# Optimization experiments

Hardware: AMD Instinct MI355X
Metric: run time of the kernel (lower is better)

## Reference

```python
import jax, jax.numpy as jnp
import numpy as np

N_NODES = 50000
N_EDGES = 800000
IN_C = 128
HID = 128
OUT_C = 64
N_GRAPHS = 256


def setup_inputs() -> dict:
    key = jax.random.key(0)
    ks = jax.random.split(key, 12)
    x = jax.random.normal(ks[0], (N_NODES, IN_C), dtype=jnp.float32)
    edge_index = jax.random.randint(ks[1], (2, N_EDGES), 0, N_NODES, dtype=jnp.int32)
    batch = jnp.sort(jax.random.randint(ks[2], (N_NODES,), 0, N_GRAPHS, dtype=jnp.int32))
    def lin(k, fan_in, fan_out):
        bound = 1.0 / np.sqrt(fan_in)
        kw, kb = jax.random.split(k)
        W = jax.random.uniform(kw, (fan_in, fan_out), minval=-bound, maxval=bound, dtype=jnp.float32)
        b = jax.random.uniform(kb, (fan_out,), minval=-bound, maxval=bound, dtype=jnp.float32)
        return W, b
    W1a, b1a = lin(ks[3], IN_C, HID)
    W1b, b1b = lin(ks[4], HID, HID)
    W2a, b2a = lin(ks[5], HID, HID)
    W2b, b2b = lin(ks[6], HID, HID)
    Wl, bl = lin(ks[7], HID, OUT_C)
    return {"x": x, "edge_index": edge_index, "batch": batch,
            "W1a": W1a, "b1a": b1a, "W1b": W1b, "b1b": b1b,
            "W2a": W2a, "b2a": b2a, "W2b": W2b, "b2b": b2b,
            "Wl": Wl, "bl": bl}


def gin_conv(x, edge_index, Wa, ba, Wb, bb):
    # GINConv with eps=0: h_i = MLP(x_i + sum_{j->i} x_j)
    src, dst = edge_index[0], edge_index[1]
    agg = jax.ops.segment_sum(x[src], dst, num_segments=x.shape[0])  # [N, d]
    h = x + agg
    h = jax.nn.relu(h @ Wa + ba) @ Wb + bb
    return h


def reference(x, edge_index, batch, W1a, b1a, W1b, b1b, W2a, b2a, W2b, b2b, Wl, bl):
    h = gin_conv(x, edge_index, W1a, b1a, W1b, b1b)
    h = gin_conv(h, edge_index, W2a, b2a, W2b, b2b)
    # global mean pool over graphs in the batch
    sums = jax.ops.segment_sum(h, batch, num_segments=N_GRAPHS)          # [G, HID]
    cnts = jax.ops.segment_sum(jnp.ones((h.shape[0],), h.dtype), batch, num_segments=N_GRAPHS)
    pooled = sums / jnp.maximum(cnts, 1.0)[:, None]
    return pooled @ Wl + bl  # [G, OUT_C]
```

## Files before the change

### kernel.cpp

```cpp
#include <hip/hip_runtime.h>

constexpr int N  = 50000;
constexpr int E  = 800000;
constexpr int C  = 128;
constexpr int G  = 256;
constexpr int OC = 64;
constexpr int D  = 64;

constexpr int NBUCK = 196;
constexpr int BCAP  = 5120;
constexpr int EPB = 2048;
constexpr int EB  = (E + EPB - 1) / EPB;
constexpr int WB1 = 64;
constexpr int WXB = 64;
constexpr int WHB = 32;
constexpr int GB  = (N + 255) / 256;
constexpr int FB  = NBUCK;
constexpr int MB  = (N + 63) / 64;

typedef __attribute__((ext_vector_type(8))) short short8;
typedef __attribute__((ext_vector_type(4))) float f32x4;
typedef __attribute__((ext_vector_type(2))) float f32x2;

__device__ __forceinline__ unsigned int au(float f) { return __float_as_uint(f); }

__device__ __forceinline__ unsigned short f2bf(float f) {
    unsigned int u = au(f);
    u += 0x7fffu + ((u >> 16) & 1u);
    return (unsigned short)(u >> 16);
}
__device__ __forceinline__ unsigned int pack_bf16(float lo, float hi) {
    return ((au(hi) + 0x8000u) & 0xFFFF0000u) | ((au(lo) + 0x8000u) >> 16);
}

__device__ __forceinline__ void acc16(f32x2* a, uint4 v) {
    a[0] += __builtin_amdgcn_cvt_pk_f32_fp8((int)v.x, false);
    a[1] += __builtin_amdgcn_cvt_pk_f32_fp8((int)v.x, true);
    a[2] += __builtin_amdgcn_cvt_pk_f32_fp8((int)v.y, false);
    a[3] += __builtin_amdgcn_cvt_pk_f32_fp8((int)v.y, true);
    a[4] += __builtin_amdgcn_cvt_pk_f32_fp8((int)v.z, false);
    a[5] += __builtin_amdgcn_cvt_pk_f32_fp8((int)v.z, true);
    a[6] += __builtin_amdgcn_cvt_pk_f32_fp8((int)v.w, false);
    a[7] += __builtin_amdgcn_cvt_pk_f32_fp8((int)v.w, true);
}
__device__ __forceinline__ void set16(f32x2* a, uint4 v) {
    a[0] = __builtin_amdgcn_cvt_pk_f32_fp8((int)v.x, false);
    a[1] = __builtin_amdgcn_cvt_pk_f32_fp8((int)v.x, true);
    a[2] = __builtin_amdgcn_cvt_pk_f32_fp8((int)v.y, false);
    a[3] = __builtin_amdgcn_cvt_pk_f32_fp8((int)v.y, true);
    a[4] = __builtin_amdgcn_cvt_pk_f32_fp8((int)v.z, false);
    a[5] = __builtin_amdgcn_cvt_pk_f32_fp8((int)v.z, true);
    a[6] = __builtin_amdgcn_cvt_pk_f32_fp8((int)v.w, false);
    a[7] = __builtin_amdgcn_cvt_pk_f32_fp8((int)v.w, true);
}

__device__ __forceinline__ void gather_rows(f32x2* a, const uint4* F16,
                                            const unsigned short* irow, int dg, int l) {
    const uint2* i2 = (const uint2*)irow;
    int nb  = dg >> 2;
    int rem = dg & 3;
    if (nb > 0) {
        uint2 iu = i2[0];
        int t0 = (int)(iu.x & 0xffffu), t1 = (int)(iu.x >> 16);
        int t2 = (int)(iu.y & 0xffffu), t3 = (int)(iu.y >> 16);
        uint4 v0 = F16[(size_t)t0 * 8 + l];
        uint4 v1 = F16[(size_t)t1 * 8 + l];
        uint4 v2 = F16[(size_t)t2 * 8 + l];
        uint4 v3 = F16[(size_t)t3 * 8 + l];
        for (int b = 1; b < nb; ++b) {
            uint2 ju = i2[b];
            int u0 = (int)(ju.x & 0xffffu), u1 = (int)(ju.x >> 16);
            int u2 = (int)(ju.y & 0xffffu), u3 = (int)(ju.y >> 16);
            uint4 w0 = F16[(size_t)u0 * 8 + l];
            uint4 w1 = F16[(size_t)u1 * 8 + l];
            uint4 w2 = F16[(size_t)u2 * 8 + l];
            uint4 w3 = F16[(size_t)u3 * 8 + l];
            acc16(a, v0); acc16(a, v1); acc16(a, v2); acc16(a, v3);
            v0 = w0; v1 = w1; v2 = w2; v3 = w3;
        }
        acc16(a, v0); acc16(a, v1); acc16(a, v2); acc16(a, v3);
    }
    if (rem) {
        const unsigned short* ir = irow + nb * 4;
#pragma unroll
        for (int m = 0; m < 3; ++m) {
            if (m < rem) {
                uint4 v = F16[(size_t)ir[m] * 8 + l];
                acc16(a, v);
            }
        }
    }
}

__device__ __forceinline__ void tile_sort(short* sorted, const int* deg, int row0,
                                          int lane, int wave) {
    if (wave == 0) {
        int n0 = row0 + lane;
        int key = (n0 < N) ? min(deg[n0], D) : -1;
        int rank = 0;
        for (int j = 0; j < 64; ++j) {
            int kj = __shfl(key, j);
            rank += (kj < key) || (kj == key && j < lane);
        }
        sorted[rank] = (short)lane;
    }
}


__global__ __launch_bounds__(256) void build_prep_kernel(const int* __restrict__ src,
                                                         const int* __restrict__ dst,
                                                         int* __restrict__ bcount,
                                                         unsigned int* __restrict__ bucketbuf,
                                                         const float* __restrict__ W1a,
                                                         const float* __restrict__ W1b,
                                                         const float* __restrict__ W2a,
                                                         const float* __restrict__ W2b,
                                                         const float* __restrict__ Wl,
                                                         const float* __restrict__ bl,
                                                         const float* __restrict__ b1b,
                                                         const float* __restrict__ b2b,
                                                         unsigned short* __restrict__ wt1a,
                                                         unsigned short* __restrict__ wtx,
                                                         float* __restrict__ Whead,
                                                         float* __restrict__ c1,
                                                         float* __restrict__ bhead,
                                                         const int* __restrict__ batch,
                                                         int* __restrict__ gcnt) {
    int b = blockIdx.x;
    int tid = threadIdx.x;
    if (b < EB) {
        __shared__ int lcount[NBUCK];
        __shared__ int lbase[NBUCK];
        __shared__ int lcur[NBUCK];
        for (int i = tid; i < NBUCK; i += 256) { lcount[i] = 0; lcur[i] = 0; }
        __syncthreads();
        int e0 = b * EPB;
        int sv[8], dv[8];
#pragma unroll
        for (int i = 0; i < 8; ++i) {
            int e = e0 + i * 256 + tid;
            if (e < E) {
                sv[i] = src[e];
                dv[i] = dst[e];
                atomicAdd(&lcount[dv[i] >> 8], 1);
            } else {
                dv[i] = -1;
            }
        }
        __syncthreads();
        if (tid < NBUCK) {
            int c = lcount[tid];
            lbase[tid] = (c > 0) ? atomicAdd(&bcount[tid], c) : 0;
        }
        __syncthreads();
#pragma unroll
        for (int i = 0; i < 8; ++i) {
            if (dv[i] >= 0) {
                int bk = dv[i] >> 8;
                int pos = lbase[bk] + atomicAdd(&lcur[bk], 1);
                if (pos < BCAP)
                    bucketbuf[(size_t)bk * BCAP + pos] =
                        ((unsigned int)sv[i] << 16) | (unsigned int)(dv[i] & 255);
            }
        }
    } else if (b < EB + WB1) {
        int idx = (b - EB) * 256 + tid;
        int n = idx >> 7, k = idx & 127;
        wt1a[idx] = f2bf(W1a[k * 128 + n]);
    } else if (b < EB + WB1 + WXB) {
        int idx = (b - EB - WB1) * 256 + tid;
        int i = idx >> 7, j = idx & 127;
        float acc = 0.f;
        for (int k = 0; k < 128; ++k) acc += W1b[i * 128 + k] * W2a[k * 128 + j];
        wtx[j * 128 + i] = f2bf(acc);
    } else if (b < EB + WB1 + WXB + WHB) {
        int idx = (b - EB - WB1 - WXB) * 256 + tid;
        int i = idx >> 6, j = idx & 63;
        float acc = 0.f;
        for (int k = 0; k < 128; ++k) acc += W2b[i * 128 + k] * Wl[k * OC + j];
        Whead[i * OC + j] = acc;
    } else if (b == EB + WB1 + WXB + WHB) {
        if (tid < 128) {
            float acc = 0.f;
            for (int k = 0; k < 128; ++k) acc += b1b[k] * W2a[k * 128 + tid];
            c1[tid] = acc;
        } else if (tid < 192) {
            int j = tid - 128;
            float acc = bl[j];
            for (int k = 0; k < 128; ++k) acc += b2b[k] * Wl[k * OC + j];
            bhead[j] = acc;
        }
    } else {
        __shared__ int h[G];
        h[tid] = 0;
        __syncthreads();
        int i = (b - (EB + WB1 + WXB + WHB + 1)) * 256 + tid;
        if (i < N) atomicAdd(&h[batch[i]], 1);
        __syncthreads();
        int c = h[tid];
        if (c > 0) atomicAdd(&gcnt[tid], c);
    }
}


__global__ __launch_bounds__(512, 6) void mid_kernel(const int* __restrict__ bcount,
                                                     const unsigned int* __restrict__ bucketbuf,
                                                     unsigned short* __restrict__ ell,
                                                     int* __restrict__ deg,
                                                     const float* __restrict__ x,
                                                     const unsigned short* __restrict__ wt1a,
                                                     unsigned char* __restrict__ z1) {
    int tid = threadIdx.x;
    if (blockIdx.x < FB) {
        __shared__ int lcur[256];
        int b = blockIdx.x;
        if (tid < 256) lcur[tid] = 0;
        __syncthreads();
        int cnt = min(bcount[b], BCAP);
        const unsigned int* buf = bucketbuf + (size_t)b * BCAP;
        int nbase = b << 8;
        for (int i = tid; i < cnt; i += 512) {
            unsigned int e = buf[i];
            int dlow = (int)(e & 255u);
            int p = atomicAdd(&lcur[dlow], 1);
            if (p < D) ell[(size_t)(nbase + dlow) * D + p] = (unsigned short)(e >> 16);
        }
        __syncthreads();
        if (tid < 256) {
            int node = nbase + tid;
            if (node < N) deg[node] = lcur[tid];
        }
        return;
    }
    constexpr int LD = 136;
    __shared__ short Xl[64 * LD];
    __shared__ short Wl[128 * LD];
    int lane = tid & 63, wave = tid >> 6;
    int row0 = (blockIdx.x - FB) * 64;

    const short8* Wg = (const short8*)wt1a;
#pragma unroll
    for (int i = tid; i < 2048; i += 512) {
        int r = i >> 4, c = i & 15;
        *((short8*)(Wl + r * LD) + c) = Wg[i];
    }
    const float4* x4 = (const float4*)(x + (size_t)row0 * C);
#pragma unroll
    for (int i = tid; i < 2048; i += 512) {
        int r = i >> 5, c4 = i & 31;
        float4 v = (row0 + r < N) ? x4[i] : make_float4(0.f, 0.f, 0.f, 0.f);
        uint2 u;
        u.x = pack_bf16(v.x, v.y);
        u.y = pack_bf16(v.z, v.w);
        *(uint2*)(Xl + r * LD + c4 * 4) = u;
    }

    int mw = wave >> 2, nw = wave & 3;
    int lid = lane & 15, quad = lane >> 4;
    f32x4 acc[2][2];
#pragma unroll
    for (int nt = 0; nt < 2; ++nt) {
        acc[0][nt] = (f32x4){0.f, 0.f, 0.f, 0.f};
        acc[1][nt] = (f32x4){0.f, 0.f, 0.f, 0.f};
    }
    __syncthreads();

#pragma unroll
    for (int ks = 0; ks < 4; ++ks) {
        short8 a0 = *(const short8*)(Xl + (mw * 32 + lid) * LD + ks * 32 + quad * 8);
        short8 a1 = *(const short8*)(Xl + (mw * 32 + 16 + lid) * LD + ks * 32 + quad * 8);
#pragma unroll
        for (int nt = 0; nt < 2; ++nt) {
            short8 bf = *(const short8*)(Wl + (nw * 32 + nt * 16 + lid) * LD + ks * 32 + quad * 8);
            acc[0][nt] = __builtin_amdgcn_mfma_f32_16x16x32_bf16(a0, bf, acc[0][nt], 0, 0, 0);
            acc[1][nt] = __builtin_amdgcn_mfma_f32_16x16x32_bf16(a1, bf, acc[1][nt], 0, 0, 0);
        }
    }

#pragma unroll
    for (int mt = 0; mt < 2; ++mt) {
#pragma unroll
        for (int nt = 0; nt < 2; ++nt) {
            int mbase = row0 + mw * 32 + mt * 16 + quad * 4;
            int n = nw * 32 + nt * 16 + lid;
            f32x4 v = acc[mt][nt];
#pragma unroll
            for (int r = 0; r < 4; ++r) {
                int row = mbase + r;
                if (row < N) {
                    unsigned int p = (unsigned int)__builtin_amdgcn_cvt_pk_fp8_f32(v[r], 0.f, 0, false);
                    z1[(size_t)row * 128 + n] = (unsigned char)(p & 0xFF);
                }
            }
        }
    }
}


__global__ __launch_bounds__(512, 6) void k2_kernel(const unsigned char* __restrict__ z1,
                                                    const int* __restrict__ deg,
                                                    const unsigned short* __restrict__ ell,
                                                    const unsigned short* __restrict__ wtx,
                                                    const float* __restrict__ b1a,
                                                    unsigned char* __restrict__ z2) {
    constexpr int LD = 136;
    __shared__ short Xl[64 * LD];
    __shared__ short Wl[128 * LD];
    __shared__ short sorted[64];
    int tid = threadIdx.x;
    int lane = tid & 63, wave = tid >> 6;
    int row0 = blockIdx.x * 64;

    const short8* Wg = (const short8*)wtx;
#pragma unroll
    for (int i = tid; i < 2048; i += 512) {
        int r = i >> 4, c = i & 15;
        *((short8*)(Wl + r * LD) + c) = Wg[i];
    }
    tile_sort(sorted, deg, row0, lane, wave);
    __syncthreads();

    {
        int grp = tid >> 3;
        int l   = tid & 7;
        int lr  = sorted[grp];
        const uint4* F16 = (const uint4*)z1;
        int n = row0 + lr;
        f32x2 a[8];
        if (n < N) {
            int dgc = min(deg[n], D);
            set16(a, F16[(size_t)n * 8 + l]);
            gather_rows(a, F16, ell + (size_t)n * D, dgc, l);
            const f32x2* bp = (const f32x2*)(b1a + l * 16);
#pragma unroll
            for (int q = 0; q < 8; ++q) {
                a[q] += bp[q];
                a[q].x = fmaxf(a[q].x, 0.f);
                a[q].y = fmaxf(a[q].y, 0.f);
            }
        } else {
#pragma unroll
            for (int q = 0; q < 8; ++q) a[q] = (f32x2){0.f, 0.f};
        }
        uint4 o0, o1;
        o0.x = pack_bf16(a[0].x, a[0].y); o0.y = pack_bf16(a[1].x, a[1].y);
        o0.z = pack_bf16(a[2].x, a[2].y); o0.w = pack_bf16(a[3].x, a[3].y);
        o1.x = pack_bf16(a[4].x, a[4].y); o1.y = pack_bf16(a[5].x, a[5].y);
        o1.z = pack_bf16(a[6].x, a[6].y); o1.w = pack_bf16(a[7].x, a[7].y);
        uint4* xp = (uint4*)(Xl + lr * LD + l * 16);
        xp[0] = o0;
        xp[1] = o1;
    }

    int mw = wave >> 2, nw = wave & 3;
    int lid = lane & 15, quad = lane >> 4;
    f32x4 acc[2][2];
#pragma unroll
    for (int nt = 0; nt < 2; ++nt) {
        acc[0][nt] = (f32x4){0.f, 0.f, 0.f, 0.f};
        acc[1][nt] = (f32x4){0.f, 0.f, 0.f, 0.f};
    }
    __syncthreads();

#pragma unroll
    for (int ks = 0; ks < 4; ++ks) {
        short8 a0 = *(const short8*)(Xl + (mw * 32 + lid) * LD + ks * 32 + quad * 8);
        short8 a1 = *(const short8*)(Xl + (mw * 32 + 16 + lid) * LD + ks * 32 + quad * 8);
#pragma unroll
        for (int nt = 0; nt < 2; ++nt) {
            short8 bf = *(const short8*)(Wl + (nw * 32 + nt * 16 + lid) * LD + ks * 32 + quad * 8);
            acc[0][nt] = __builtin_amdgcn_mfma_f32_16x16x32_bf16(a0, bf, acc[0][nt], 0, 0, 0);
            acc[1][nt] = __builtin_amdgcn_mfma_f32_16x16x32_bf16(a1, bf, acc[1][nt], 0, 0, 0);
        }
    }

#pragma unroll
    for (int mt = 0; mt < 2; ++mt) {
#pragma unroll
        for (int nt = 0; nt < 2; ++nt) {
            int mbase = row0 + mw * 32 + mt * 16 + quad * 4;
            int n = nw * 32 + nt * 16 + lid;
            f32x4 v = acc[mt][nt];
#pragma unroll
            for (int r = 0; r < 4; ++r) {
                int row = mbase + r;
                if (row < N) {
                    unsigned int p = (unsigned int)__builtin_amdgcn_cvt_pk_fp8_f32(v[r], 0.f, 0, false);
                    z2[(size_t)row * 128 + n] = (unsigned char)(p & 0xFF);
                }
            }
        }
    }
}


__global__ __launch_bounds__(512, 6) void k3_kernel(const unsigned char* __restrict__ z2,
                                                    const int* __restrict__ deg,
                                                    const unsigned short* __restrict__ ell,
                                                    const float* __restrict__ c1,
                                                    const float* __restrict__ b2a,
                                                    const int* __restrict__ batch,
                                                    float* __restrict__ gsum) {
    constexpr int LD = 136;
    __shared__ short Xl[64 * LD];
    __shared__ short sorted[64];
    int tid = threadIdx.x;
    int lane = tid & 63, wave = tid >> 6;
    int row0 = blockIdx.x * 64;

    tile_sort(sorted, deg, row0, lane, wave);
    __syncthreads();

    {
        int grp = tid >> 3;
        int l   = tid & 7;
        int lr  = sorted[grp];
        const uint4* F16 = (const uint4*)z2;
        int n = row0 + lr;
        f32x2 a[8];
        if (n < N) {
            int dfull = deg[n];
            int dgc = min(dfull, D);
            set16(a, F16[(size_t)n * 8 + l]);
            gather_rows(a, F16, ell + (size_t)n * D, dgc, l);
            float degf = (float)(1 + dfull);
            const f32x2* c1p = (const f32x2*)(c1 + l * 16);
            const f32x2* b2p = (const f32x2*)(b2a + l * 16);
#pragma unroll
            for (int q = 0; q < 8; ++q) {
                a[q] += degf * c1p[q] + b2p[q];
                a[q].x = fmaxf(a[q].x, 0.f);
                a[q].y = fmaxf(a[q].y, 0.f);
            }
        } else {
#pragma unroll
            for (int q = 0; q < 8; ++q) a[q] = (f32x2){0.f, 0.f};
        }
        uint4 o0, o1;
        o0.x = pack_bf16(a[0].x, a[0].y); o0.y = pack_bf16(a[1].x, a[1].y);
        o0.z = pack_bf16(a[2].x, a[2].y); o0.w = pack_bf16(a[3].x, a[3].y);
        o1.x = pack_bf16(a[4].x, a[4].y); o1.y = pack_bf16(a[5].x, a[5].y);
        o1.z = pack_bf16(a[6].x, a[6].y); o1.w = pack_bf16(a[7].x, a[7].y);
        uint4* xp = (uint4*)(Xl + lr * LD + l * 16);
        xp[0] = o0;
        xp[1] = o1;
    }
    __syncthreads();

    int r0 = wave * 8;
    int gprev = -1;
    float a0 = 0.f, a1 = 0.f;
    for (int rr = 0; rr < 8; ++rr) {
        int row = row0 + r0 + rr;
        if (row >= N) break;
        int g = batch[row];
        if (g != gprev) {
            if (gprev >= 0) {
                atomicAdd(&gsum[gprev * C + 2 * lane], a0);
                atomicAdd(&gsum[gprev * C + 2 * lane + 1], a1);
            }
            gprev = g; a0 = 0.f; a1 = 0.f;
        }
        unsigned int pv = *(const unsigned int*)(Xl + (r0 + rr) * LD + 2 * lane);
        a0 += __uint_as_float((pv & 0xffffu) << 16);
        a1 += __uint_as_float(pv & 0xffff0000u);
    }
    if (gprev >= 0) {
        atomicAdd(&gsum[gprev * C + 2 * lane], a0);
        atomicAdd(&gsum[gprev * C + 2 * lane + 1], a1);
    }
}


__global__ __launch_bounds__(64) void head_kernel(const float* __restrict__ gsum,
                                                  const int* __restrict__ gcnt,
                                                  const float* __restrict__ Whead,
                                                  const float* __restrict__ bhead,
                                                  float* __restrict__ out) {
    int g = blockIdx.x;
    int t = threadIdx.x;
    __shared__ float pooled[C];
    float inv = 1.0f / (float)max(gcnt[g], 1);
    pooled[t]      = gsum[g * C + t] * inv;
    pooled[t + 64] = gsum[g * C + 64 + t] * inv;
    __syncthreads();
    float o = bhead[t];
#pragma unroll 4
    for (int k = 0; k < C; ++k) o += pooled[k] * Whead[k * OC + t];
    out[g * OC + t] = o;
}


extern "C" void kernel_launch(void* const* d_in, const int* in_sizes, int n_in,
                              void* d_out, int out_size, void* d_ws, size_t ws_size,
                              hipStream_t stream) {
    const float* x    = (const float*)d_in[0];
    const int*   ei   = (const int*)d_in[1];
    const int*   bat  = (const int*)d_in[2];
    const float* W1a  = (const float*)d_in[3];
    const float* b1a  = (const float*)d_in[4];
    const float* W1b  = (const float*)d_in[5];
    const float* b1b  = (const float*)d_in[6];
    const float* W2a  = (const float*)d_in[7];
    const float* b2a  = (const float*)d_in[8];
    const float* W2b  = (const float*)d_in[9];
    const float* b2b  = (const float*)d_in[10];
    const float* Wl   = (const float*)d_in[11];
    const float* bl   = (const float*)d_in[12];
    float*       out  = (float*)d_out;

    float* gsum    = (float*)d_ws;
    int*   gcnt    = (int*)(gsum + G * C);
    int*   bcount  = gcnt + G;
    int*   deg     = bcount + NBUCK;
    unsigned int*   bucketbuf = (unsigned int*)(deg + N);
    unsigned short* ell  = (unsigned short*)(bucketbuf + (size_t)NBUCK * BCAP);
    unsigned short* wt1a = ell + (size_t)N * D;
    unsigned short* wtx  = wt1a + 16384;
    float* Whead = (float*)(wtx + 16384);
    float* c1    = Whead + 128 * OC;
    float* bhead = c1 + 128;
    unsigned char* z1 = (unsigned char*)(bhead + OC);
    unsigned char* z2 = z1 + (size_t)N * 128;

    const int* src = ei;
    const int* dst = ei + E;

    hipMemsetAsync(gsum, 0, (size_t)(G * C + G + NBUCK) * sizeof(int), stream);

    build_prep_kernel<<<EB + WB1 + WXB + WHB + 1 + GB, 256, 0, stream>>>(
        src, dst, bcount, bucketbuf, W1a, W1b, W2a, W2b, Wl, bl, b1b, b2b,
        wt1a, wtx, Whead, c1, bhead, bat, gcnt);

    mid_kernel<<<FB + MB, 512, 0, stream>>>(bcount, bucketbuf, ell, deg,
                                            x, wt1a, z1);

    k2_kernel<<<MB, 512, 0, stream>>>(z1, deg, ell, wtx, b1a, z2);
    k3_kernel<<<MB, 512, 0, stream>>>(z2, deg, ell, c1, b2a, bat, gsum);
    head_kernel<<<G, 64, 0, stream>>>(gsum, gcnt, Whead, bhead, out);
}
```

Before: 191.1 us.

## Split fp8 node features into two 64-channel planes for cache-friendlier gathers

Stores the fp8 intermediate features z1/z2 as two planes of 64 channels each instead of row-major 128-byte rows. The neighbor gather in k2/k3 now runs one pass per plane, with 8-byte loads per lane and 8 neighbors in flight. The aim is to halve the working set of each gather pass (3.2 MB per plane) so it stays resident in L2/LLC and random-access misses drop. In exchange the ELL index list is read twice and the gathers become narrower and more numerous, and the MFMA epilogue writes become more strided.

```diff
diff --git a/kernel.cpp b/kernel.cpp
--- a/kernel.cpp
+++ b/kernel.cpp
@@ -33,60 +33,67 @@
     return ((au(hi) + 0x8000u) & 0xFFFF0000u) | ((au(lo) + 0x8000u) >> 16);
 }
 
-__device__ __forceinline__ void acc16(f32x2* a, uint4 v) {
+__device__ __forceinline__ void acc8(f32x2* a, uint2 v) {
     a[0] += __builtin_amdgcn_cvt_pk_f32_fp8((int)v.x, false);
     a[1] += __builtin_amdgcn_cvt_pk_f32_fp8((int)v.x, true);
     a[2] += __builtin_amdgcn_cvt_pk_f32_fp8((int)v.y, false);
     a[3] += __builtin_amdgcn_cvt_pk_f32_fp8((int)v.y, true);
-    a[4] += __builtin_amdgcn_cvt_pk_f32_fp8((int)v.z, false);
-    a[5] += __builtin_amdgcn_cvt_pk_f32_fp8((int)v.z, true);
-    a[6] += __builtin_amdgcn_cvt_pk_f32_fp8((int)v.w, false);
-    a[7] += __builtin_amdgcn_cvt_pk_f32_fp8((int)v.w, true);
-}
-__device__ __forceinline__ void set16(f32x2* a, uint4 v) {
+}
+__device__ __forceinline__ void set8(f32x2* a, uint2 v) {
     a[0] = __builtin_amdgcn_cvt_pk_f32_fp8((int)v.x, false);
     a[1] = __builtin_amdgcn_cvt_pk_f32_fp8((int)v.x, true);
     a[2] = __builtin_amdgcn_cvt_pk_f32_fp8((int)v.y, false);
     a[3] = __builtin_amdgcn_cvt_pk_f32_fp8((int)v.y, true);
-    a[4] = __builtin_amdgcn_cvt_pk_f32_fp8((int)v.z, false);
-    a[5] = __builtin_amdgcn_cvt_pk_f32_fp8((int)v.z, true);
-    a[6] = __builtin_amdgcn_cvt_pk_f32_fp8((int)v.w, false);
-    a[7] = __builtin_amdgcn_cvt_pk_f32_fp8((int)v.w, true);
-}
-
-__device__ __forceinline__ void gather_rows(f32x2* a, const uint4* F16,
-                                            const unsigned short* irow, int dg, int l) {
-    const uint2* i2 = (const uint2*)irow;
-    int nb  = dg >> 2;
-    int rem = dg & 3;
+}
+
+__device__ __forceinline__ void gather_plane(f32x2* a, const uint2* P,
+                                             const unsigned short* irow, int dg, int l) {
+    const uint4* i8 = (const uint4*)irow;
+    int nb  = dg >> 3;
+    int rem = dg & 7;
     if (nb > 0) {
-        uint2 iu = i2[0];
+        uint4 iu = i8[0];
         int t0 = (int)(iu.x & 0xffffu), t1 = (int)(iu.x >> 16);
         int t2 = (int)(iu.y & 0xffffu), t3 = (int)(iu.y >> 16);
-        uint4 v0 = F16[(size_t)t0 * 8 + l];
-        uint4 v1 = F16[(size_t)t1 * 8 + l];
-        uint4 v2 = F16[(size_t)t2 * 8 + l];
-        uint4 v3 = F16[(size_t)t3 * 8 + l];
+        int t4 = (int)(iu.z & 0xffffu), t5 = (int)(iu.z >> 16);
+        int t6 = (int)(iu.w & 0xffffu), t7 = (int)(iu.w >> 16);
+        uint2 v0 = P[(size_t)t0 * 8 + l];
+        uint2 v1 = P[(size_t)t1 * 8 + l];
+        uint2 v2 = P[(size_t)t2 * 8 + l];
+        uint2 v3 = P[(size_t)t3 * 8 + l];
+        uint2 v4 = P[(size_t)t4 * 8 + l];
+        uint2 v5 = P[(size_t)t5 * 8 + l];
+        uint2 v6 = P[(size_t)t6 * 8 + l];
+        uint2 v7 = P[(size_t)t7 * 8 + l];
         for (int b = 1; b < nb; ++b) {
-            uint2 ju = i2[b];
+            uint4 ju = i8[b];
             int u0 = (int)(ju.x & 0xffffu), u1 = (int)(ju.x >> 16);
             int u2 = (int)(ju.y & 0xffffu), u3 = (int)(ju.y >> 16);
-            uint4 w0 = F16[(size_t)u0 * 8 + l];
-            uint4 w1 = F16[(size_t)u1 * 8 + l];
-            uint4 w2 = F16[(size_t)u2 * 8 + l];
-            uint4 w3 = F16[(size_t)u3 * 8 + l];
-            acc16(a, v0); acc16(a, v1); acc16(a, v2); acc16(a, v3);
+            int u4 = (int)(ju.z & 0xffffu), u5 = (int)(ju.z >> 16);
+            int u6 = (int)(ju.w & 0xffffu), u7 = (int)(ju.w >> 16);
+            uint2 w0 = P[(size_t)u0 * 8 + l];
+            uint2 w1 = P[(size_t)u1 * 8 + l];
+            uint2 w2 = P[(size_t)u2 * 8 + l];
+            uint2 w3 = P[(size_t)u3 * 8 + l];
+            uint2 w4 = P[(size_t)u4 * 8 + l];
+            uint2 w5 = P[(size_t)u5 * 8 + l];
+            uint2 w6 = P[(size_t)u6 * 8 + l];
+            uint2 w7 = P[(size_t)u7 * 8 + l];
+            acc8(a, v0); acc8(a, v1); acc8(a, v2); acc8(a, v3);
+            acc8(a, v4); acc8(a, v5); acc8(a, v6); acc8(a, v7);
             v0 = w0; v1 = w1; v2 = w2; v3 = w3;
-        }
-        acc16(a, v0); acc16(a, v1); acc16(a, v2); acc16(a, v3);
+            v4 = w4; v5 = w5; v6 = w6; v7 = w7;
+        }
+        acc8(a, v0); acc8(a, v1); acc8(a, v2); acc8(a, v3);
+        acc8(a, v4); acc8(a, v5); acc8(a, v6); acc8(a, v7);
     }
     if (rem) {
-        const unsigned short* ir = irow + nb * 4;
-#pragma unroll
-        for (int m = 0; m < 3; ++m) {
+        const unsigned short* ir = irow + nb * 8;
+#pragma unroll
+        for (int m = 0; m < 7; ++m) {
             if (m < rem) {
-                uint4 v = F16[(size_t)ir[m] * 8 + l];
-                acc16(a, v);
+                uint2 v = P[(size_t)ir[m] * 8 + l];
+                acc8(a, v);
             }
         }
     }
@@ -283,13 +290,14 @@
         for (int nt = 0; nt < 2; ++nt) {
             int mbase = row0 + mw * 32 + mt * 16 + quad * 4;
             int n = nw * 32 + nt * 16 + lid;
+            size_t pbase = (size_t)(n >> 6) * N * 64 + (n & 63);
             f32x4 v = acc[mt][nt];
 #pragma unroll
             for (int r = 0; r < 4; ++r) {
                 int row = mbase + r;
                 if (row < N) {
                     unsigned int p = (unsigned int)__builtin_amdgcn_cvt_pk_fp8_f32(v[r], 0.f, 0, false);
-                    z1[(size_t)row * 128 + n] = (unsigned char)(p & 0xFF);
+                    z1[pbase + (size_t)row * 64] = (unsigned char)(p & 0xFF);
                 }
             }
         }
@@ -324,32 +332,32 @@
         int grp = tid >> 3;
         int l   = tid & 7;
         int lr  = sorted[grp];
-        const uint4* F16 = (const uint4*)z1;
         int n = row0 + lr;
-        f32x2 a[8];
-        if (n < N) {
-            int dgc = min(deg[n], D);
-            set16(a, F16[(size_t)n * 8 + l]);
-            gather_rows(a, F16, ell + (size_t)n * D, dgc, l);
-            const f32x2* bp = (const f32x2*)(b1a + l * 16);
-#pragma unroll
-            for (int q = 0; q < 8; ++q) {
-                a[q] += bp[q];
-                a[q].x = fmaxf(a[q].x, 0.f);
-                a[q].y = fmaxf(a[q].y, 0.f);
-            }
-        } else {
-#pragma unroll
-            for (int q = 0; q < 8; ++q) a[q] = (f32x2){0.f, 0.f};
-        }
-        uint4 o0, o1;
-        o0.x = pack_bf16(a[0].x, a[0].y); o0.y = pack_bf16(a[1].x, a[1].y);
-        o0.z = pack_bf16(a[2].x, a[2].y); o0.w = pack_bf16(a[3].x, a[3].y);
-        o1.x = pack_bf16(a[4].x, a[4].y); o1.y = pack_bf16(a[5].x, a[5].y);
-        o1.z = pack_bf16(a[6].x, a[6].y); o1.w = pack_bf16(a[7].x, a[7].y);
-        uint4* xp = (uint4*)(Xl + lr * LD + l * 16);
-        xp[0] = o0;
-        xp[1] = o1;
+        int dgc = (n < N) ? min(deg[n], D) : 0;
+        const unsigned short* irow = ell + (size_t)n * D;
+#pragma unroll 1
+        for (int p = 0; p < 2; ++p) {
+            const uint2* P = (const uint2*)(z1 + (size_t)p * N * 64);
+            f32x2 a[4];
+            if (n < N) {
+                set8(a, P[(size_t)n * 8 + l]);
+                gather_plane(a, P, irow, dgc, l);
+                const f32x2* bp = (const f32x2*)(b1a + p * 64 + l * 8);
+#pragma unroll
+                for (int q = 0; q < 4; ++q) {
+                    a[q] += bp[q];
+                    a[q].x = fmaxf(a[q].x, 0.f);
+                    a[q].y = fmaxf(a[q].y, 0.f);
+                }
+            } else {
+#pragma unroll
+                for (int q = 0; q < 4; ++q) a[q] = (f32x2){0.f, 0.f};
+            }
+            uint4 o;
+            o.x = pack_bf16(a[0].x, a[0].y); o.y = pack_bf16(a[1].x, a[1].y);
+            o.z = pack_bf16(a[2].x, a[2].y); o.w = pack_bf16(a[3].x, a[3].y);
+            *(uint4*)(Xl + lr * LD + p * 64 + l * 8) = o;
+        }
     }
 
     int mw = wave >> 2, nw = wave & 3;
@@ -380,13 +388,14 @@
         for (int nt = 0; nt < 2; ++nt) {
             int mbase = row0 + mw * 32 + mt * 16 + quad * 4;
             int n = nw * 32 + nt * 16 + lid;
+            size_t pbase = (size_t)(n >> 6) * N * 64 + (n & 63);
             f32x4 v = acc[mt][nt];
 #pragma unroll
             for (int r = 0; r < 4; ++r) {
                 int row = mbase + r;
                 if (row < N) {
                     unsigned int p = (unsigned int)__builtin_amdgcn_cvt_pk_fp8_f32(v[r], 0.f, 0, false);
-                    z2[(size_t)row * 128 + n] = (unsigned char)(p & 0xFF);
+                    z2[pbase + (size_t)row * 64] = (unsigned char)(p & 0xFF);
                 }
             }
         }
@@ -415,35 +424,35 @@
         int grp = tid >> 3;
         int l   = tid & 7;
         int lr  = sorted[grp];
-        const uint4* F16 = (const uint4*)z2;
         int n = row0 + lr;
-        f32x2 a[8];
-        if (n < N) {
-            int dfull = deg[n];
-            int dgc = min(dfull, D);
-            set16(a, F16[(size_t)n * 8 + l]);
-            gather_rows(a, F16, ell + (size_t)n * D, dgc, l);
-            float degf = (float)(1 + dfull);
-            const f32x2* c1p = (const f32x2*)(c1 + l * 16);
-            const f32x2* b2p = (const f32x2*)(b2a + l * 16);
-#pragma unroll
-            for (int q = 0; q < 8; ++q) {
-                a[q] += degf * c1p[q] + b2p[q];
-                a[q].x = fmaxf(a[q].x, 0.f);
-                a[q].y = fmaxf(a[q].y, 0.f);
-            }
-        } else {
-#pragma unroll
-            for (int q = 0; q < 8; ++q) a[q] = (f32x2){0.f, 0.f};
-        }
-        uint4 o0, o1;
-        o0.x = pack_bf16(a[0].x, a[0].y); o0.y = pack_bf16(a[1].x, a[1].y);
-        o0.z = pack_bf16(a[2].x, a[2].y); o0.w = pack_bf16(a[3].x, a[3].y);
-        o1.x = pack_bf16(a[4].x, a[4].y); o1.y = pack_bf16(a[5].x, a[5].y);
-        o1.z = pack_bf16(a[6].x, a[6].y); o1.w = pack_bf16(a[7].x, a[7].y);
-        uint4* xp = (uint4*)(Xl + lr * LD + l * 16);
-        xp[0] = o0;
-        xp[1] = o1;
+        int dfull = (n < N) ? deg[n] : 0;
+        int dgc = min(dfull, D);
+        float degf = (float)(1 + dfull);
+        const unsigned short* irow = ell + (size_t)n * D;
+#pragma unroll 1
+        for (int p = 0; p < 2; ++p) {
+            const uint2* P = (const uint2*)(z2 + (size_t)p * N * 64);
+            f32x2 a[4];
+            if (n < N) {
+                set8(a, P[(size_t)n * 8 + l]);
+                gather_plane(a, P, irow, dgc, l);
+                const f32x2* c1p = (const f32x2*)(c1 + p * 64 + l * 8);
+                const f32x2* b2p = (const f32x2*)(b2a + p * 64 + l * 8);
+#pragma unroll
+                for (int q = 0; q < 4; ++q) {
+                    a[q] += degf * c1p[q] + b2p[q];
+                    a[q].x = fmaxf(a[q].x, 0.f);
+                    a[q].y = fmaxf(a[q].y, 0.f);
+                }
+            } else {
+#pragma unroll
+                for (int q = 0; q < 4; ++q) a[q] = (f32x2){0.f, 0.f};
+            }
+            uint4 o;
+            o.x = pack_bf16(a[0].x, a[0].y); o.y = pack_bf16(a[1].x, a[1].y);
+            o.z = pack_bf16(a[2].x, a[2].y); o.w = pack_bf16(a[3].x, a[3].y);
+            *(uint4*)(Xl + lr * LD + p * 64 + l * 8) = o;
+        }
     }
     __syncthreads();
 
@@ -521,7 +530,7 @@
     float* c1    = Whead + 128 * OC;
     float* bhead = c1 + 128;
     unsigned char* z1 = (unsigned char*)(bhead + OC);
-    unsigned char* z2 = z1 + (size_t)N * 128;
+    unsigned char* z2 = z1 + (size_t)2 * N * 64;
 
     const int* src = ei;
     const int* dst = ei + E;
```

New measurement: 208.7 us. 1.09x slower.

## Move first-layer GEMM into build kernel and split bucket fill into own kernel

Applied to the files above, without the earlier changes.

The x·W1a GEMM blocks now run inside the edge-bucketing prep kernel, so the dense GEMM overlaps with edge binning instead of running after it. The bucket-to-ELL fill becomes a small standalone kernel. Each GEMM block converts W1a to bf16 in shared memory itself, dropping the separate wt1a transpose pass at the cost of redundant per-block weight conversion. The prep kernel moves to 512 threads with a shared smem buffer, and the gather loop prefetches the next index pair one iteration early.

```diff
diff --git a/kernel.cpp b/kernel.cpp
--- a/kernel.cpp
+++ b/kernel.cpp
@@ -11,12 +11,10 @@
 constexpr int BCAP  = 5120;
 constexpr int EPB = 2048;
 constexpr int EB  = (E + EPB - 1) / EPB;
-constexpr int WB1 = 64;
-constexpr int WXB = 64;
-constexpr int WHB = 32;
-constexpr int GB  = (N + 255) / 256;
-constexpr int FB  = NBUCK;
 constexpr int MB  = (N + 63) / 64;
+constexpr int WXB = 32;
+constexpr int WHB = 16;
+constexpr int GB  = (N + 511) / 512;
 
 typedef __attribute__((ext_vector_type(8))) short short8;
 typedef __attribute__((ext_vector_type(4))) float f32x4;
@@ -67,14 +65,16 @@
         uint4 v1 = F16[(size_t)t1 * 8 + l];
         uint4 v2 = F16[(size_t)t2 * 8 + l];
         uint4 v3 = F16[(size_t)t3 * 8 + l];
+        uint2 jn;
+        if (nb > 1) jn = i2[1];
         for (int b = 1; b < nb; ++b) {
-            uint2 ju = i2[b];
-            int u0 = (int)(ju.x & 0xffffu), u1 = (int)(ju.x >> 16);
-            int u2 = (int)(ju.y & 0xffffu), u3 = (int)(ju.y >> 16);
+            int u0 = (int)(jn.x & 0xffffu), u1 = (int)(jn.x >> 16);
+            int u2 = (int)(jn.y & 0xffffu), u3 = (int)(jn.y >> 16);
             uint4 w0 = F16[(size_t)u0 * 8 + l];
             uint4 w1 = F16[(size_t)u1 * 8 + l];
             uint4 w2 = F16[(size_t)u2 * 8 + l];
             uint4 w3 = F16[(size_t)u3 * 8 + l];
+            if (b + 1 < nb) jn = i2[b + 1];
             acc16(a, v0); acc16(a, v1); acc16(a, v2); acc16(a, v3);
             v0 = w0; v1 = w1; v2 = w2; v3 = w3;
         }
@@ -107,38 +107,41 @@
 }
 
 
-__global__ __launch_bounds__(256) void build_prep_kernel(const int* __restrict__ src,
-                                                         const int* __restrict__ dst,
-                                                         int* __restrict__ bcount,
-                                                         unsigned int* __restrict__ bucketbuf,
-                                                         const float* __restrict__ W1a,
-                                                         const float* __restrict__ W1b,
-                                                         const float* __restrict__ W2a,
-                                                         const float* __restrict__ W2b,
-                                                         const float* __restrict__ Wl,
-                                                         const float* __restrict__ bl,
-                                                         const float* __restrict__ b1b,
-                                                         const float* __restrict__ b2b,
-                                                         unsigned short* __restrict__ wt1a,
-                                                         unsigned short* __restrict__ wtx,
-                                                         float* __restrict__ Whead,
-                                                         float* __restrict__ c1,
-                                                         float* __restrict__ bhead,
-                                                         const int* __restrict__ batch,
-                                                         int* __restrict__ gcnt) {
+__global__ __launch_bounds__(512, 6) void build_prep_kernel(const int* __restrict__ src,
+                                                            const int* __restrict__ dst,
+                                                            int* __restrict__ bcount,
+                                                            unsigned int* __restrict__ bucketbuf,
+                                                            const float* __restrict__ W1a,
+                                                            const float* __restrict__ W1b,
+                                                            const float* __restrict__ W2a,
+                                                            const float* __restrict__ W2b,
+                                                            const float* __restrict__ Wlin,
+                                                            const float* __restrict__ bl,
+                                                            const float* __restrict__ b1b,
+                                                            const float* __restrict__ b2b,
+                                                            unsigned short* __restrict__ wtx,
+                                                            float* __restrict__ Whead,
+                                                            float* __restrict__ c1,
+                                                            float* __restrict__ bhead,
+                                                            const int* __restrict__ batch,
+                                                            int* __restrict__ gcnt,
+                                                            const float* __restrict__ x,
+                                                            unsigned char* __restrict__ z1) {
+    constexpr int LD = 136;
+    __shared__ __attribute__((aligned(16))) char smem[64 * LD * 2 + 128 * LD * 2];
     int b = blockIdx.x;
     int tid = threadIdx.x;
     if (b < EB) {
-        __shared__ int lcount[NBUCK];
-        __shared__ int lbase[NBUCK];
-        __shared__ int lcur[NBUCK];
-        for (int i = tid; i < NBUCK; i += 256) { lcount[i] = 0; lcur[i] = 0; }
+        int* lcount = (int*)smem;
+        int* lbase  = lcount + NBUCK;
+        int* lcur   = lbase + NBUCK;
+        if (tid < NBUCK) { lcount[tid] = 0; lcur[tid] = 0; }
         __syncthreads();
         int e0 = b * EPB;
-        int sv[8], dv[8];
-#pragma unroll
-        for (int i = 0; i < 8; ++i) {
-            int e = e0 + i * 256 + tid;
+        int sv[4], dv[4];
+#pragma unroll
+        for (int i = 0; i < 4; ++i) {
+            int e = e0 + i * 512 + tid;
             if (e < E) {
                 sv[i] = src[e];
                 dv[i] = dst[e];
@@ -154,7 +157,7 @@
         }
         __syncthreads();
 #pragma unroll
-        for (int i = 0; i < 8; ++i) {
+        for (int i = 0; i < 4; ++i) {
             if (dv[i] >= 0) {
                 int bk = dv[i] >> 8;
                 int pos = lbase[bk] + atomicAdd(&lcur[bk], 1);
@@ -163,23 +166,78 @@
                         ((unsigned int)sv[i] << 16) | (unsigned int)(dv[i] & 255);
             }
         }
-    } else if (b < EB + WB1) {
-        int idx = (b - EB) * 256 + tid;
-        int n = idx >> 7, k = idx & 127;
-        wt1a[idx] = f2bf(W1a[k * 128 + n]);
-    } else if (b < EB + WB1 + WXB) {
-        int idx = (b - EB - WB1) * 256 + tid;
+    } else if (b < EB + MB) {
+        short* Xl = (short*)smem;
+        short* Wl = (short*)smem + 64 * LD;
+        int lane = tid & 63, wave = tid >> 6;
+        int row0 = (b - EB) * 64;
+
+        for (int i = tid; i < 16384; i += 512) {
+            int k = i >> 7, n = i & 127;
+            Wl[n * LD + k] = (short)f2bf(W1a[i]);
+        }
+        const float4* x4 = (const float4*)(x + (size_t)row0 * C);
+        for (int i = tid; i < 2048; i += 512) {
+            int r = i >> 5, c4 = i & 31;
+            float4 v = (row0 + r < N) ? x4[i] : make_float4(0.f, 0.f, 0.f, 0.f);
+            uint2 u;
+            u.x = pack_bf16(v.x, v.y);
+            u.y = pack_bf16(v.z, v.w);
+            *(uint2*)(Xl + r * LD + c4 * 4) = u;
+        }
+
+        int mw = wave >> 2, nw = wave & 3;
+        int lid = lane & 15, quad = lane >> 4;
+        f32x4 acc[2][2];
+#pragma unroll
+        for (int nt = 0; nt < 2; ++nt) {
+            acc[0][nt] = (f32x4){0.f, 0.f, 0.f, 0.f};
+            acc[1][nt] = (f32x4){0.f, 0.f, 0.f, 0.f};
+        }
+        __syncthreads();
+
+#pragma unroll
+        for (int ks = 0; ks < 4; ++ks) {
+            short8 a0 = *(const short8*)(Xl + (mw * 32 + lid) * LD + ks * 32 + quad * 8);
+            short8 a1 = *(const short8*)(Xl + (mw * 32 + 16 + lid) * LD + ks * 32 + quad * 8);
+#pragma unroll
+            for (int nt = 0; nt < 2; ++nt) {
+                short8 bf = *(const short8*)(Wl + (nw * 32 + nt * 16 + lid) * LD + ks * 32 + quad * 8);
+                acc[0][nt] = __builtin_amdgcn_mfma_f32_16x16x32_bf16(a0, bf, acc[0][nt], 0, 0, 0);
+                acc[1][nt] = __builtin_amdgcn_mfma_f32_16x16x32_bf16(a1, bf, acc[1][nt], 0, 0, 0);
+            }
+        }
+
+#pragma unroll
+        for (int mt = 0; mt < 2; ++mt) {
+#pragma unroll
+            for (int nt = 0; nt < 2; ++nt) {
+                int mbase = row0 + mw * 32 + mt * 16 + quad * 4;
+                int n = nw * 32 + nt * 16 + lid;
+                f32x4 v = acc[mt][nt];
+#pragma unroll
+                for (int r = 0; r < 4; ++r) {
+                    int row = mbase + r;
+                    if (row < N) {
+                        unsigned int p = (unsigned int)__builtin_amdgcn_cvt_pk_fp8_f32(v[r], 0.f, 0, false);
+                        z1[(size_t)row * 128 + n] = (unsigned char)(p & 0xFF);
+                    }
+                }
+            }
+        }
+    } else if (b < EB + MB + WXB) {
+        int idx = (b - EB - MB) * 512 + tid;
         int i = idx >> 7, j = idx & 127;
         float acc = 0.f;
         for (int k = 0; k < 128; ++k) acc += W1b[i * 128 + k] * W2a[k * 128 + j];
         wtx[j * 128 + i] = f2bf(acc);
-    } else if (b < EB + WB1 + WXB + WHB) {
-        int idx = (b - EB - WB1 - WXB) * 256 + tid;
+    } else if (b < EB + MB + WXB + WHB) {
+        int idx = (b - EB - MB - WXB) * 512 + tid;
         int i = idx >> 6, j = idx & 63;
         float acc = 0.f;
-        for (int k = 0; k < 128; ++k) acc += W2b[i * 128 + k] * Wl[k * OC + j];
+        for (int k = 0; k < 128; ++k) acc += W2b[i * 128 + k] * Wlin[k * OC + j];
         Whead[i * OC + j] = acc;
-    } else if (b == EB + WB1 + WXB + WHB) {
+    } else if (b == EB + MB + WXB + WHB) {
         if (tid < 128) {
             float acc = 0.f;
             for (int k = 0; k < 128; ++k) acc += b1b[k] * W2a[k * 128 + tid];
@@ -187,112 +245,46 @@
         } else if (tid < 192) {
             int j = tid - 128;
             float acc = bl[j];
-            for (int k = 0; k < 128; ++k) acc += b2b[k] * Wl[k * OC + j];
+            for (int k = 0; k < 128; ++k) acc += b2b[k] * Wlin[k * OC + j];
             bhead[j] = acc;
         }
     } else {
-        __shared__ int h[G];
-        h[tid] = 0;
+        int* h = (int*)smem;
+        if (tid < G) h[tid] = 0;
         __syncthreads();
-        int i = (b - (EB + WB1 + WXB + WHB + 1)) * 256 + tid;
+        int i = (b - (EB + MB + WXB + WHB + 1)) * 512 + tid;
         if (i < N) atomicAdd(&h[batch[i]], 1);
         __syncthreads();
-        int c = h[tid];
-        if (c > 0) atomicAdd(&gcnt[tid], c);
-    }
-}
-
-
-__global__ __launch_bounds__(512, 6) void mid_kernel(const int* __restrict__ bcount,
-                                                     const unsigned int* __restrict__ bucketbuf,
-                                                     unsigned short* __restrict__ ell,
-                                                     int* __restrict__ deg,
-                                                     const float* __restrict__ x,
-                                                     const unsigned short* __restrict__ wt1a,
-                                                     unsigned char* __restrict__ z1) {
+        if (tid < G) {
+            int c = h[tid];
+            if (c > 0) atomicAdd(&gcnt[tid], c);
+        }
+    }
+}
+
+
+__global__ __launch_bounds__(512) void fill_kernel(const int* __restrict__ bcount,
+                                                   const unsigned int* __restrict__ bucketbuf,
+                                                   unsigned short* __restrict__ ell,
+                                                   int* __restrict__ deg) {
+    __shared__ int lcur[256];
+    int b = blockIdx.x;
     int tid = threadIdx.x;
-    if (blockIdx.x < FB) {
-        __shared__ int lcur[256];
-        int b = blockIdx.x;
-        if (tid < 256) lcur[tid] = 0;
-        __syncthreads();
-        int cnt = min(bcount[b], BCAP);
-        const unsigned int* buf = bucketbuf + (size_t)b * BCAP;
-        int nbase = b << 8;
-        for (int i = tid; i < cnt; i += 512) {
-            unsigned int e = buf[i];
-            int dlow = (int)(e & 255u);
-            int p = atomicAdd(&lcur[dlow], 1);
-            if (p < D) ell[(size_t)(nbase + dlow) * D + p] = (unsigned short)(e >> 16);
-        }
-        __syncthreads();
-        if (tid < 256) {
-            int node = nbase + tid;
-            if (node < N) deg[node] = lcur[tid];
-        }
-        return;
-    }
-    constexpr int LD = 136;
-    __shared__ short Xl[64 * LD];
-    __shared__ short Wl[128 * LD];
-    int lane = tid & 63, wave = tid >> 6;
-    int row0 = (blockIdx.x - FB) * 64;
-
-    const short8* Wg = (const short8*)wt1a;
-#pragma unroll
-    for (int i = tid; i < 2048; i += 512) {
-        int r = i >> 4, c = i & 15;
-        *((short8*)(Wl + r * LD) + c) = Wg[i];
-    }
-    const float4* x4 = (const float4*)(x + (size_t)row0 * C);
-#pragma unroll
-    for (int i = tid; i < 2048; i += 512) {
-        int r = i >> 5, c4 = i & 31;
-        float4 v = (row0 + r < N) ? x4[i] : make_float4(0.f, 0.f, 0.f, 0.f);
-        uint2 u;
-        u.x = pack_bf16(v.x, v.y);
-        u.y = pack_bf16(v.z, v.w);
-        *(uint2*)(Xl + r * LD + c4 * 4) = u;
-    }
-
-    int mw = wave >> 2, nw = wave & 3;
-    int lid = lane & 15, quad = lane >> 4;
-    f32x4 acc[2][2];
-#pragma unroll
-    for (int nt = 0; nt < 2; ++nt) {
-        acc[0][nt] = (f32x4){0.f, 0.f, 0.f, 0.f};
-        acc[1][nt] = (f32x4){0.f, 0.f, 0.f, 0.f};
-    }
-    __syncthreads();
-
-#pragma unroll
-    for (int ks = 0; ks < 4; ++ks) {
-        short8 a0 = *(const short8*)(Xl + (mw * 32 + lid) * LD + ks * 32 + quad * 8);
-        short8 a1 = *(const short8*)(Xl + (mw * 32 + 16 + lid) * LD + ks * 32 + quad * 8);
-#pragma unroll
-        for (int nt = 0; nt < 2; ++nt) {
-            short8 bf = *(const short8*)(Wl + (nw * 32 + nt * 16 + lid) * LD + ks * 32 + quad * 8);
-            acc[0][nt] = __builtin_amdgcn_mfma_f32_16x16x32_bf16(a0, bf, acc[0][nt], 0, 0, 0);
-            acc[1][nt] = __builtin_amdgcn_mfma_f32_16x16x32_bf16(a1, bf, acc[1][nt], 0, 0, 0);
-        }
-    }
-
-#pragma unroll
-    for (int mt = 0; mt < 2; ++mt) {
-#pragma unroll
-        for (int nt = 0; nt < 2; ++nt) {
-            int mbase = row0 + mw * 32 + mt * 16 + quad * 4;
-            int n = nw * 32 + nt * 16 + lid;
-            f32x4 v = acc[mt][nt];
-#pragma unroll
-            for (int r = 0; r < 4; ++r) {
-                int row = mbase + r;
-                if (row < N) {
-                    unsigned int p = (unsigned int)__builtin_amdgcn_cvt_pk_fp8_f32(v[r], 0.f, 0, false);
-                    z1[(size_t)row * 128 + n] = (unsigned char)(p & 0xFF);
-                }
-            }
-        }
+    if (tid < 256) lcur[tid] = 0;
+    __syncthreads();
+    int cnt = min(bcount[b], BCAP);
+    const unsigned int* buf = bucketbuf + (size_t)b * BCAP;
+    int nbase = b << 8;
+    for (int i = tid; i < cnt; i += 512) {
+        unsigned int e = buf[i];
+        int dlow = (int)(e & 255u);
+        int p = atomicAdd(&lcur[dlow], 1);
+        if (p < D) ell[(size_t)(nbase + dlow) * D + p] = (unsigned short)(e >> 16);
+    }
+    __syncthreads();
+    if (tid < 256) {
+        int node = nbase + tid;
+        if (node < N) deg[node] = lcur[tid];
     }
 }
 
@@ -515,8 +507,7 @@
     int*   deg     = bcount + NBUCK;
     unsigned int*   bucketbuf = (unsigned int*)(deg + N);
     unsigned short* ell  = (unsigned short*)(bucketbuf + (size_t)NBUCK * BCAP);
-    unsigned short* wt1a = ell + (size_t)N * D;
-    unsigned short* wtx  = wt1a + 16384;
+    unsigned short* wtx  = ell + (size_t)N * D;
     float* Whead = (float*)(wtx + 16384);
     float* c1    = Whead + 128 * OC;
     float* bhead = c1 + 128;
@@ -528,12 +519,11 @@
 
     hipMemsetAsync(gsum, 0, (size_t)(G * C + G + NBUCK) * sizeof(int), stream);
 
-    build_prep_kernel<<<EB + WB1 + WXB + WHB + 1 + GB, 256, 0, stream>>>(
+    build_prep_kernel<<<EB + MB + WXB + WHB + 1 + GB, 512, 0, stream>>>(
         src, dst, bcount, bucketbuf, W1a, W1b, W2a, W2b, Wl, bl, b1b, b2b,
-        wt1a, wtx, Whead, c1, bhead, bat, gcnt);
-
-    mid_kernel<<<FB + MB, 512, 0, stream>>>(bcount, bucketbuf, ell, deg,
-                                            x, wt1a, z1);
+        wtx, Whead, c1, bhead, bat, gcnt, x, z1);
+
+    fill_kernel<<<NBUCK, 512, 0, stream>>>(bcount, bucketbuf, ell, deg);
 
     k2_kernel<<<MB, 512, 0, stream>>>(z1, deg, ell, wtx, b1a, z2);
     k3_kernel<<<MB, 512, 0, stream>>>(z2, deg, ell, c1, b2a, bat, gsum);
```

Result: no change. 194.2 us (+1.6%).
